# Optimization experiments

Measured on AMD Instinct MI355X. Metric: run time of the kernel, lower is better.

## Reference

```python
import jax, jax.numpy as jnp
import numpy as np

B, N = 512, 128
K = 3                      # top-k per row/col
CONF_THRESH = 0.05
ACCEPT_RADIUS = 0.1
CORR_THRESHOLD = 3         # min correspondences per patch
CORR_LIMIT = 2048          # verification-set size (correspondence_limit)
NUM_REFINE = 5
EPS = 1e-5


def setup_inputs() -> dict:
    key = jax.random.key(0)
    k1, k2, k3, k4, k5 = jax.random.split(key, 5)
    return {
        'score_mat': jax.random.normal(k1, (B, N, N), dtype=jnp.float32),
        'ref_knn_points': jax.random.normal(k2, (B, N, 3), dtype=jnp.float32),
        'src_knn_points': jax.random.normal(k3, (B, N, 3), dtype=jnp.float32),
        'ref_knn_masks': jax.random.bernoulli(k4, 0.95, (B, N)),
        'src_knn_masks': jax.random.bernoulli(k5, 0.95, (B, N)),
    }


def _svd_transform(H, src_c, ref_c):
    """H: (..., 3, 3) covariance; src_c/ref_c: (..., 3) centroids -> (..., 4, 4)."""
    U, _, Vh = jnp.linalg.svd(H)
    V = jnp.swapaxes(Vh, -1, -2)
    Ut = jnp.swapaxes(U, -1, -2)
    d = jnp.sign(jnp.linalg.det(V @ Ut))
    E = jnp.zeros_like(H).at[..., 0, 0].set(1.0).at[..., 1, 1].set(1.0).at[..., 2, 2].set(d)
    R = V @ E @ Ut
    t = ref_c - jnp.einsum('...ij,...j->...i', R, src_c)
    T = jnp.zeros(H.shape[:-2] + (4, 4), H.dtype)
    T = T.at[..., :3, :3].set(R).at[..., :3, 3].set(t).at[..., 3, 3].set(1.0)
    return T


def weighted_procrustes(src, ref, w):
    """src/ref: (C, 3), w: (C,) -> (4, 4). weight_thresh=0, weights >= 0 so no clamp."""
    wn = w / (jnp.sum(w, axis=-1, keepdims=True) + EPS)
    sc = jnp.einsum('n,nc->c', wn, src)
    rc = jnp.einsum('n,nc->c', wn, ref)
    H = jnp.einsum('nc,n,nd->cd', src - sc, wn, ref - rc)
    return _svd_transform(H, sc, rc)


def _topk_mask_last(scores):
    """Keep top-K values along the last axis of (B, R, S), zeros elsewhere."""
    vals, idx = jax.lax.top_k(scores, K)
    b = jnp.arange(scores.shape[0])[:, None, None]
    r = jnp.arange(scores.shape[1])[None, :, None]
    return jnp.zeros_like(scores).at[b, r, idx].set(vals)


def reference(score_mat, ref_knn_points, src_knn_points, ref_knn_masks, src_knn_masks):
    scores = jnp.exp(score_mat)  # score_mat holds log-scores (GeoTransformer forward)

    # --- correspondence matrix: dual top-k scatter + mutual + valid masks ---
    ref_corr = _topk_mask_last(scores) > CONF_THRESH
    src_corr = jnp.swapaxes(_topk_mask_last(jnp.swapaxes(scores, 1, 2)), 1, 2) > CONF_THRESH
    corr = ref_corr & src_corr  # mutual=True
    corr = corr & (ref_knn_masks[:, :, None] & src_knn_masks[:, None, :])

    masked = scores * corr.astype(scores.dtype)  # (B, N, N)
    patch_count = jnp.sum(corr, axis=(1, 2))      # correspondences per patch

    # --- per-patch weighted procrustes over all (n, m) pairs, zero-weighted pads ---
    wn = masked / (jnp.sum(masked, axis=(1, 2), keepdims=True) + EPS)
    sc = jnp.einsum('bnm,bmc->bc', wn, src_knn_points)
    rc = jnp.einsum('bnm,bnc->bc', wn, ref_knn_points)
    Hb = jnp.einsum('bnm,bmc,bnd->bcd', wn, src_knn_points - sc[:, None, :], ref_knn_points - rc[:, None, :])
    # gradients cannot flow past the boolean inlier masks below; stop_gradient avoids
    # spurious NaNs from degenerate 3x3 SVD backward on empty patches
    local_T = jax.lax.stop_gradient(_svd_transform(Hb, sc, rc))  # (B, 4, 4)

    # --- verification set: global top CORR_LIMIT correspondences ---
    flat = masked.reshape(-1)
    sel_scores, sel_idx = jax.lax.top_k(flat, CORR_LIMIT)
    b_i = sel_idx // (N * N)
    r_i = (sel_idx % (N * N)) // N
    s_i = sel_idx % N
    ref_c = ref_knn_points[b_i, r_i]  # (C, 3)
    src_c = src_knn_points[b_i, s_i]  # (C, 3)
    valid = sel_scores > 0

    # --- score every local transform by inlier count on the verification set ---
    R_all = local_T[:, :3, :3]
    t_all = local_T[:, :3, 3]
    aligned = jnp.einsum('pij,cj->pci', R_all, src_c) + t_all[:, None, :]  # (B, C, 3)
    resid = jnp.linalg.norm(ref_c[None] - aligned, axis=-1)
    inlier = (resid < ACCEPT_RADIUS) & valid[None]
    counts = jnp.where(patch_count >= CORR_THRESHOLD, jnp.sum(inlier, axis=-1), -1)
    best = jnp.argmax(counts)
    cur = sel_scores * inlier[best].astype(sel_scores.dtype)

    # --- global refinement: iterative re-weighted procrustes ---
    T = weighted_procrustes(src_c, ref_c, cur)
    for _ in range(NUM_REFINE - 1):
        aligned1 = src_c @ T[:3, :3].T + T[:3, 3]
        r1 = jnp.linalg.norm(ref_c - aligned1, axis=-1)
        cur = sel_scores * (r1 < ACCEPT_RADIUS).astype(sel_scores.dtype)
        T = weighted_procrustes(src_c, ref_c, cur)
    return T
```

## Files before the change

### kernel.cpp

```cpp
#include <hip/hip_runtime.h>
#include <math.h>

#define BB 512
#define NN 128
#define CAND_CAP (512*384)
#define LIMIT 2048
#define EQCAP 16384
#define NBIN1 4096

__device__ inline bool read_mask(const void* p, int i, int mode){
  if (mode == 0) return ((const int*)p)[i] != 0;
  if (mode == 1) return ((const unsigned char*)p)[i] != 0;
  return ((const float*)p)[i] != 0.0f;
}

__device__ inline float fast_rcp(float x){ return __builtin_amdgcn_rcpf(x); }
__device__ inline float fast_rsq(float x){ return __builtin_amdgcn_rsqf(x); }

__device__ __forceinline__ void kabsch9(
    float h00, float h01, float h02,
    float h10, float h11, float h12,
    float h20, float h21, float h22,
    float& r00, float& r01, float& r02,
    float& r10, float& r11, float& r12,
    float& r20, float& r21, float& r22)
{
  float s00 = h00*h00 + h10*h10 + h20*h20;
  float s01 = h00*h01 + h10*h11 + h20*h21;
  float s02 = h00*h02 + h10*h12 + h20*h22;
  float s11 = h01*h01 + h11*h11 + h21*h21;
  float s12 = h01*h02 + h11*h12 + h21*h22;
  float s22 = h02*h02 + h12*h12 + h22*h22;
  float v00=1.f,v01=0.f,v02=0.f, v10=0.f,v11=1.f,v12=0.f, v20=0.f,v21=0.f,v22=1.f;
  for (int sweep = 0; sweep < 10; sweep++){
    float off  = s01*s01 + s02*s02 + s12*s12;
    float base = s00*s00 + s11*s11 + s22*s22;
    if (off <= base*1e-14f + 1e-36f) break;
    if (fabsf(s01) > 1e-30f){
      float tau = (s11 - s00) * fast_rcp(2.f*s01);
      float tt  = (tau >= 0.f ? 1.f : -1.f) * fast_rcp(fabsf(tau) + sqrtf(1.f + tau*tau));
      float c = fast_rsq(1.f + tt*tt), s = tt*c;
      float n00 = c*c*s00 - 2.f*c*s*s01 + s*s*s11;
      float n11 = s*s*s00 + 2.f*c*s*s01 + c*c*s11;
      float n02 = c*s02 - s*s12;
      float n12 = s*s02 + c*s12;
      s00=n00; s11=n11; s01=0.f; s02=n02; s12=n12;
      float a,b;
      a=v00; b=v01; v00=c*a-s*b; v01=s*a+c*b;
      a=v10; b=v11; v10=c*a-s*b; v11=s*a+c*b;
      a=v20; b=v21; v20=c*a-s*b; v21=s*a+c*b;
    }
    if (fabsf(s02) > 1e-30f){
      float tau = (s22 - s00) * fast_rcp(2.f*s02);
      float tt  = (tau >= 0.f ? 1.f : -1.f) * fast_rcp(fabsf(tau) + sqrtf(1.f + tau*tau));
      float c = fast_rsq(1.f + tt*tt), s = tt*c;
      float n00 = c*c*s00 - 2.f*c*s*s02 + s*s*s22;
      float n22 = s*s*s00 + 2.f*c*s*s02 + c*c*s22;
      float n01 = c*s01 - s*s12;
      float n12 = s*s01 + c*s12;
      s00=n00; s22=n22; s02=0.f; s01=n01; s12=n12;
      float a,b;
      a=v00; b=v02; v00=c*a-s*b; v02=s*a+c*b;
      a=v10; b=v12; v10=c*a-s*b; v12=s*a+c*b;
      a=v20; b=v22; v20=c*a-s*b; v22=s*a+c*b;
    }
    if (fabsf(s12) > 1e-30f){
      float tau = (s22 - s11) * fast_rcp(2.f*s12);
      float tt  = (tau >= 0.f ? 1.f : -1.f) * fast_rcp(fabsf(tau) + sqrtf(1.f + tau*tau));
      float c = fast_rsq(1.f + tt*tt), s = tt*c;
      float n11 = c*c*s11 - 2.f*c*s*s12 + s*s*s22;
      float n22 = s*s*s11 + 2.f*c*s*s12 + c*c*s22;
      float n01 = c*s01 - s*s02;
      float n02 = s*s01 + c*s02;
      s11=n11; s22=n22; s12=0.f; s01=n01; s02=n02;
      float a,b;
      a=v01; b=v02; v01=c*a-s*b; v02=s*a+c*b;
      a=v11; b=v12; v11=c*a-s*b; v12=s*a+c*b;
      a=v21; b=v22; v21=c*a-s*b; v22=s*a+c*b;
    }
  }
  float l0=s00, l1=s11, l2=s22;
  float a0=v00, a1=v10, a2=v20;
  float b0=v01, b1=v11, b2=v21;
  float c0=v02, c1=v12, c2=v22;
  if (l0 < l1){ float x; x=l0;l0=l1;l1=x; x=a0;a0=b0;b0=x; x=a1;a1=b1;b1=x; x=a2;a2=b2;b2=x; }
  if (l0 < l2){ float x; x=l0;l0=l2;l2=x; x=a0;a0=c0;c0=x; x=a1;a1=c1;c1=x; x=a2;a2=c2;c2=x; }
  if (l1 < l2){ float x; x=l1;l1=l2;l2=x; x=b0;b0=c0;c0=x; x=b1;b1=c1;c1=x; x=b2;b2=c2;c2=x; }
  float sig0 = sqrtf(fmaxf(l0, 0.f));
  if (!(sig0 > 1e-12f)){
    r00=1.f; r01=0.f; r02=0.f; r10=0.f; r11=1.f; r12=0.f; r20=0.f; r21=0.f; r22=1.f;
    return;
  }
  float u0x = h00*a0 + h01*a1 + h02*a2;
  float u0y = h10*a0 + h11*a1 + h12*a2;
  float u0z = h20*a0 + h21*a1 + h22*a2;
  float in0 = fast_rsq(u0x*u0x + u0y*u0y + u0z*u0z);
  u0x *= in0; u0y *= in0; u0z *= in0;
  float u1x = h00*b0 + h01*b1 + h02*b2;
  float u1y = h10*b0 + h11*b1 + h12*b2;
  float u1z = h20*b0 + h21*b1 + h22*b2;
  float dp = u1x*u0x + u1y*u0y + u1z*u0z;
  u1x -= dp*u0x; u1y -= dp*u0y; u1z -= dp*u0z;
  float d1 = u1x*u1x + u1y*u1y + u1z*u1z;
  if (sqrtf(d1) > sig0*1e-5f){
    float in1 = fast_rsq(d1);
    u1x *= in1; u1y *= in1; u1z *= in1;
  } else {
    float au0 = fabsf(u0x), au1 = fabsf(u0y), au2 = fabsf(u0z);
    float e0 = 0.f, e1 = 0.f, e2 = 0.f;
    if (au0 <= au1 && au0 <= au2) e0 = 1.f; else if (au1 <= au2) e1 = 1.f; else e2 = 1.f;
    float d2 = e0*u0x + e1*u0y + e2*u0z;
    u1x = e0 - d2*u0x; u1y = e1 - d2*u0y; u1z = e2 - d2*u0z;
    float nn = fast_rsq(u1x*u1x + u1y*u1y + u1z*u1z);
    u1x *= nn; u1y *= nn; u1z *= nn;
  }
  float u2x = u0y*u1z - u0z*u1y;
  float u2y = u0z*u1x - u0x*u1z;
  float u2z = u0x*u1y - u0y*u1x;
  float cxv = b1*c2 - b2*c1;
  float cyv = b2*c0 - b0*c2;
  float czv = b0*c1 - b1*c0;
  float detV = a0*cxv + a1*cyv + a2*czv;
  float dd = (detV >= 0.f) ? 1.f : -1.f;
  float w2x = dd*u2x, w2y = dd*u2y, w2z = dd*u2z;
  r00=a0*u0x + b0*u1x + c0*w2x;  r01=a0*u0y + b0*u1y + c0*w2y;  r02=a0*u0z + b0*u1z + c0*w2z;
  r10=a1*u0x + b1*u1x + c1*w2x;  r11=a1*u0y + b1*u1y + c1*w2y;  r12=a1*u0z + b1*u1z + c1*w2z;
  r20=a2*u0x + b2*u1x + c2*w2x;  r21=a2*u0y + b2*u1y + c2*w2y;  r22=a2*u0z + b2*u1z + c2*w2z;
}

__global__ __launch_bounds__(256) void k1_kernel(
    const float* __restrict__ score, const float* __restrict__ refp,
    const float* __restrict__ srcp, const void* __restrict__ rmaskp,
    const void* __restrict__ smaskp,
    int* hdr, float* cand_vals, int* cand_idx,
    float* Hsr, int* pcount)
{
  __shared__ float parts[2][NN][3];
  __shared__ float srcsh[NN*3];
  __shared__ float refsh[NN*3];
  __shared__ float c3sh[NN];
  __shared__ unsigned char smk[NN], rmk[NN];
  __shared__ float candv[4][96];
  __shared__ int   candi[4][96];
  __shared__ int   wcnt[4];
  __shared__ int   woff[4];
  __shared__ int   bbase;
  __shared__ float red[4][17];
  __shared__ int smode;
  const int b = blockIdx.x, t = threadIdx.x;
  const int w = t >> 6, l = t & 63;

  if (t < 64){
    unsigned v = ((const unsigned*)rmaskp)[t];
    bool n01 = !(v == 0u || v == 1u);
    bool nf  = !(v == 0u || v == 0x3F800000u);
    unsigned long long b01 = __ballot(n01), bf = __ballot(nf);
    if (t == 0) smode = (b01 == 0ull) ? 0 : ((bf == 0ull) ? 2 : 1);
  }
  if (t < 4) wcnt[t] = 0;
  for (int i = t; i < NN*3; i += 256){
    srcsh[i] = srcp[b*NN*3 + i];
    refsh[i] = refp[b*NN*3 + i];
  }

  {
    const int c = t & 127, h = t >> 7;
    float a1=-1e30f, a2=-1e30f, a3=-1e30f;
    const float* colp = score + (size_t)b*NN*NN + (size_t)(h*64)*NN + c;
#pragma unroll 8
    for (int i = 0; i < 64; i++){
      float v = colp[i*NN];
      float m = fminf(a1, v);
      a1 = fmaxf(a1, v);
      a3 = fmaxf(a3, fminf(a2, m));
      a2 = fmaxf(a2, m);
    }
    parts[h][c][0]=a1; parts[h][c][1]=a2; parts[h][c][2]=a3;
  }
  __syncthreads();
  if (t < NN){
    float a1=parts[0][t][0], a2=parts[0][t][1], a3=parts[0][t][2];
    float b1=parts[1][t][0], b2=parts[1][t][1], b3=parts[1][t][2];
    c3sh[t] = fmaxf(fmaxf(fminf(a1,b2), fminf(a2,b1)), fmaxf(a3,b3));
    int mode = smode;
    smk[t] = read_mask(smaskp, b*NN + t, mode) ? 1 : 0;
    rmk[t] = read_mask(rmaskp, b*NN + t, mode) ? 1 : 0;
  }
  __syncthreads();

  float cn0=0.f, A0=0.f, Rx0=0.f, Ry0=0.f, Rz0=0.f;
  float cn1=0.f, A1=0.f, Rx1=0.f, Ry1=0.f, Rz1=0.f;
  const float c3_0 = c3sh[l], c3_1 = c3sh[l + 64];
  const int sm0 = smk[l], sm1 = smk[l + 64];

  const float* base = score + (size_t)b*NN*NN;
  for (int rr = 0; rr < 32; rr++){
    const int r = w*32 + rr;
    const float v0 = base[r*NN + l];
    const float v1 = base[r*NN + l + 64];
    float a1 = fmaxf(v0, v1), a2 = fminf(v0, v1), a3 = -1e30f;
#pragma unroll
    for (int st = 0; st < 6; st++){
      const int mask = 1 << st;
      float o1 = __shfl_xor(a1, mask);
      float o2 = __shfl_xor(a2, mask);
      float o3 = __shfl_xor(a3, mask);
      float m1 = fmaxf(a1, o1);
      float m2 = fmaxf(fminf(a1, o1), fmaxf(a2, o2));
      float m3 = fmaxf(fmaxf(fminf(a1, o2), fminf(a2, o1)), fmaxf(a3, o3));
      a1 = m1; a2 = m2; a3 = m3;
    }
    const float r3 = a3;
    const bool rmv = rmk[r] != 0;
    const float rx = refsh[r*3+0], ry = refsh[r*3+1], rz = refsh[r*3+2];
    float e0 = 0.f, e1 = 0.f;
    bool k0 = false, k1 = false;
    if (rmv && sm0 && v0 >= r3 && v0 >= c3_0){
      e0 = expf(v0); k0 = (e0 > 0.05f);
    }
    if (rmv && sm1 && v1 >= r3 && v1 >= c3_1){
      e1 = expf(v1); k1 = (e1 > 0.05f);
    }
    if (k0){ cn0 += 1.f; A0 += e0; Rx0 += e0*rx; Ry0 += e0*ry; Rz0 += e0*rz; }
    if (k1){ cn1 += 1.f; A1 += e1; Rx1 += e1*rx; Ry1 += e1*ry; Rz1 += e1*rz; }
    unsigned long long B0 = __ballot(k0);
    unsigned long long B1 = __ballot(k1);
    int n0 = __popcll(B0), n1 = __popcll(B1);
    if (n0 + n1 > 0){
      int wb = 0;
      if (l == 0){ wb = wcnt[w]; wcnt[w] = wb + n0 + n1; }
      wb = __shfl(wb, 0);
      unsigned long long lt = (l == 0) ? 0ull : (~0ull >> (64 - l));
      if (k0){
        int pos = wb + (int)__popcll(B0 & lt);
        if (pos < 96){ candv[w][pos] = e0; candi[w][pos] = (b<<14)|(r<<7)|l; }
      }
      if (k1){
        int pos = wb + n0 + (int)__popcll(B1 & lt);
        if (pos < 96){ candv[w][pos] = e1; candi[w][pos] = (b<<14)|(r<<7)|(l+64); }
      }
    }
  }
  __syncthreads();
  if (t == 0){
    int c0 = wcnt[0] > 96 ? 96 : wcnt[0];
    int c1 = wcnt[1] > 96 ? 96 : wcnt[1];
    int c2 = wcnt[2] > 96 ? 96 : wcnt[2];
    int c3 = wcnt[3] > 96 ? 96 : wcnt[3];
    woff[0] = 0; woff[1] = c0; woff[2] = c0 + c1; woff[3] = c0 + c1 + c2;
    bbase = atomicAdd(&hdr[0], c0 + c1 + c2 + c3);
  }
  __syncthreads();
  {
    int total = wcnt[w]; if (total > 96) total = 96;
    int gbase = bbase + woff[w];
    for (int i = l; i < total; i += 64){
      int pos = gbase + i;
      if (pos < CAND_CAP){ cand_vals[pos] = candv[w][i]; cand_idx[pos] = candi[w][i]; }
    }
  }
  {
    const float sx0 = srcsh[l*3+0], sy0 = srcsh[l*3+1], sz0 = srcsh[l*3+2];
    const float sx1 = srcsh[(l+64)*3+0], sy1 = srcsh[(l+64)*3+1], sz1 = srcsh[(l+64)*3+2];
#define WSUM(VAL, IDX) { float v_ = (VAL); \
    for (int o_ = 32; o_ > 0; o_ >>= 1) v_ += __shfl_down(v_, o_); \
    if (l == 0) red[w][IDX] = v_; }
    WSUM(cn0 + cn1, 0)
    WSUM(A0 + A1, 1)
    WSUM(Rx0 + Rx1, 2)
    WSUM(Ry0 + Ry1, 3)
    WSUM(Rz0 + Rz1, 4)
    WSUM(A0*sx0 + A1*sx1, 5)
    WSUM(A0*sy0 + A1*sy1, 6)
    WSUM(A0*sz0 + A1*sz1, 7)
    WSUM(sx0*Rx0 + sx1*Rx1, 8)
    WSUM(sx0*Ry0 + sx1*Ry1, 9)
    WSUM(sx0*Rz0 + sx1*Rz1, 10)
    WSUM(sy0*Rx0 + sy1*Rx1, 11)
    WSUM(sy0*Ry0 + sy1*Ry1, 12)
    WSUM(sy0*Rz0 + sy1*Rz1, 13)
    WSUM(sz0*Rx0 + sz1*Rx1, 14)
    WSUM(sz0*Ry0 + sz1*Ry1, 15)
    WSUM(sz0*Rz0 + sz1*Rz1, 16)
#undef WSUM
  }
  __syncthreads();
  if (t == 0){
    float tot[17];
#pragma unroll
    for (int k = 0; k < 17; k++)
      tot[k] = red[0][k] + red[1][k] + red[2][k] + red[3][k];
    float Wm = tot[1];
    float denom = Wm + 1e-5f;
    float idenom = 1.f / denom;
    float s = Wm * idenom;
    float rcv[3] = { tot[2]*idenom, tot[3]*idenom, tot[4]*idenom };
    float scv[3] = { tot[5]*idenom, tot[6]*idenom, tot[7]*idenom };
    float* o = &Hsr[b*15];
#pragma unroll
    for (int c = 0; c < 3; c++)
#pragma unroll
      for (int d = 0; d < 3; d++)
        o[c*3+d] = tot[8 + c*3 + d]*idenom - (2.f - s)*scv[c]*rcv[d];
    o[9]=scv[0]; o[10]=scv[1]; o[11]=scv[2];
    o[12]=rcv[0]; o[13]=rcv[1]; o[14]=rcv[2];
    pcount[b] = (int)(tot[0] + 0.5f);
  }
}

__global__ __launch_bounds__(256) void k3a_kernel(
    const int* hdr, const float* __restrict__ cand_vals, int* hist)
{
  __shared__ int lh[NBIN1];
  int t = threadIdx.x;
  int Nc = hdr[0]; if (Nc > CAND_CAP) Nc = CAND_CAP;
  for (int j = t; j < NBIN1; j += 256) lh[j] = 0;
  __syncthreads();
  for (int i = blockIdx.x*256 + t; i < Nc; i += gridDim.x*256)
    atomicAdd(&lh[__float_as_uint(cand_vals[i]) >> 20], 1);
  __syncthreads();
  for (int j = t; j < NBIN1; j += 256)
    if (lh[j]) atomicAdd(&hist[j], lh[j]);
}

__global__ __launch_bounds__(256) void k3c_kernel(
    int* hdr, const int* __restrict__ hist,
    const float* __restrict__ cand_vals, const int* __restrict__ cand_idx,
    float* sel_vals, int* sel_idx, float* eq_vals, int* eq_idx)
{
  __shared__ int wtot[4];
  __shared__ int sb[2];
  const int t = threadIdx.x, lane = t & 63, wv = t >> 6;
  int Nc = hdr[0]; if (Nc > CAND_CAP) Nc = CAND_CAP;
  if (Nc <= LIMIT){
    if (t == 0){ sb[0] = -1; sb[1] = 0; if (blockIdx.x == 0){ hdr[4] = -1; hdr[5] = 0; } }
    __syncthreads();
  } else {
    const int chunkIdx = 255 - t;
    int csum = 0;
    for (int j = 0; j < 16; j++) csum += hist[chunkIdx*16 + j];
    int incl = csum;
    for (int off = 1; off < 64; off <<= 1){ int y = __shfl_up(incl, off); if (lane >= off) incl += y; }
    if (lane == 63) wtot[wv] = incl;
    __syncthreads();
    int wbase = 0;
    for (int w = 0; w < wv; w++) wbase += wtot[w];
    int P = wbase + incl;
    int P_prev = P - csum;
    if (P_prev < LIMIT && P >= LIMIT){
      int cum = P_prev, bin1 = chunkIdx*16, need = 0;
      for (int b2 = chunkIdx*16 + 15; b2 >= chunkIdx*16; b2--){
        int h = hist[b2];
        if (cum + h >= LIMIT){ bin1 = b2; need = LIMIT - cum; break; }
        cum += h;
      }
      sb[0] = bin1; sb[1] = need;
      if (blockIdx.x == 0){ hdr[4] = bin1; hdr[5] = need; }
    }
    __syncthreads();
  }
  int bin1 = sb[0];
  for (int i = blockIdx.x*256 + t; i < Nc; i += gridDim.x*256){
    float v = cand_vals[i];
    if (bin1 < 0){
      int p = atomicAdd(&hdr[2], 1);
      if (p < LIMIT){ sel_vals[p] = v; sel_idx[p] = cand_idx[i]; }
      continue;
    }
    int bin = (int)(__float_as_uint(v) >> 20);
    if (bin > bin1){
      int p = atomicAdd(&hdr[2], 1);
      if (p < LIMIT){ sel_vals[p] = v; sel_idx[p] = cand_idx[i]; }
    } else if (bin == bin1){
      int q = atomicAdd(&hdr[1], 1);
      if (q < EQCAP){ eq_vals[q] = v; eq_idx[q] = cand_idx[i]; }
    }
  }
}

__global__ __launch_bounds__(1024) void k3d_kernel(
    const int* hdr, const float* __restrict__ eq_vals, const int* __restrict__ eq_idx,
    float* sel_vals, int* sel_idx,
    const float* __restrict__ refp, const float* __restrict__ srcp,
    float* sel_ref, float* sel_src)
{
  __shared__ int hist[2048];
  __shared__ int eqsh[2048];
  __shared__ int wtot[16];
  __shared__ int bpair[2];
  __shared__ int sh[2];
  const int t = threadIdx.x, lane = t & 63, wv = t >> 6;
  const int bin1 = hdr[4];
  int nAbove = hdr[2]; if (nAbove > LIMIT) nAbove = LIMIT;

  auto find_boundary = [&](int need){
    int i0 = 2047 - 2*t, i1 = 2046 - 2*t;
    int g0 = hist[i0], g1 = hist[i1];
    int local = g0 + g1;
    int incl = local;
    for (int off = 1; off < 64; off <<= 1){ int y = __shfl_up(incl, off); if (lane >= off) incl += y; }
    if (lane == 63) wtot[wv] = incl;
    __syncthreads();
    int wbase = 0;
    for (int w = 0; w < wv; w++) wbase += wtot[w];
    int P_prev = wbase + incl - local;
    int P0 = P_prev + g0;
    if (P0 >= need && P_prev < need){ bpair[0] = i0; bpair[1] = need - P_prev; }
    int P1 = P0 + g1;
    if (P1 >= need && P0 < need){ bpair[0] = i1; bpair[1] = need - P0; }
    __syncthreads();
  };

  bool done = false;
  if (bin1 < 0){
    for (int i = t; i < LIMIT; i += 1024)
      if (i >= nAbove){ sel_vals[i] = 0.f; sel_idx[i] = 0; }
    done = true;
  }
  int neq = 0, need = 0;
  if (!done){
    neq = hdr[1]; if (neq > EQCAP) neq = EQCAP;
    need = hdr[5];
    if (need >= neq){
      for (int i = t; i < neq; i += 1024){ sel_vals[nAbove+i] = eq_vals[i]; sel_idx[nAbove+i] = eq_idx[i]; }
      for (int i = t; i < LIMIT; i += 1024)
        if (i >= nAbove + neq){ sel_vals[i] = 0.f; sel_idx[i] = 0; }
      done = true;
    }
  }
  if (!done){
    for (int i = t; i < 2048; i += 1024) hist[i] = 0;
    __syncthreads();
    for (int i = t; i < neq; i += 1024)
      atomicAdd(&hist[(__float_as_uint(eq_vals[i]) >> 9) & 0x7FF], 1);
    __syncthreads();
    find_boundary(need);
    int binA = bpair[0], need2 = bpair[1];
    __syncthreads();
    for (int i = t; i < 2048; i += 1024) hist[i] = 0;
    __syncthreads();
    for (int i = t; i < neq; i += 1024){
      unsigned k = __float_as_uint(eq_vals[i]);
      if ((int)((k >> 9) & 0x7FF) == binA) atomicAdd(&hist[k & 0x1FF], 1);
    }
    __syncthreads();
    find_boundary(need2);
    unsigned Tlow = (((unsigned)binA) << 9) | (unsigned)bpair[0];
    unsigned Tkey = (((unsigned)bin1) << 20) | Tlow;
    if (t == 0){ sh[0] = 0; sh[1] = 0; }
    __syncthreads();
    for (int i = t; i < neq; i += 1024){
      unsigned k = __float_as_uint(eq_vals[i]);
      unsigned k20 = k & 0xFFFFF;
      if (k20 > Tlow){
        int p = atomicAdd(&sh[0], 1);
        sel_vals[nAbove + p] = eq_vals[i]; sel_idx[nAbove + p] = eq_idx[i];
      } else if (k20 == Tlow){
        int q = atomicAdd(&sh[1], 1);
        if (q < 2048) eqsh[q] = eq_idx[i];
      }
    }
    __syncthreads();
    if (t == 0){
      int na2 = sh[0];
      int ne2 = sh[1]; if (ne2 > 2048) ne2 = 2048;
      int take = need - na2; if (take > ne2) take = ne2; if (take < 0) take = 0;
      if (nAbove + na2 + take > LIMIT) take = LIMIT - nAbove - na2;
      for (int j = 0; j < take; j++){
        int mi = j;
        for (int l2 = j+1; l2 < ne2; l2++) if (eqsh[l2] < eqsh[mi]) mi = l2;
        int tmp = eqsh[j]; eqsh[j] = eqsh[mi]; eqsh[mi] = tmp;
        sel_vals[nAbove + na2 + j] = __uint_as_float(Tkey);
        sel_idx[nAbove + na2 + j] = eqsh[j];
      }
      for (int j = nAbove + na2 + take; j < LIMIT; j++){ sel_vals[j] = 0.f; sel_idx[j] = 0; }
    }
  }
  __syncthreads();
  for (int p = t; p < LIMIT; p += 1024){
    int idx = sel_idx[p];
    int b = idx >> 14, rr = (idx >> 7) & 127, ss = idx & 127;
#pragma unroll
    for (int c = 0; c < 3; c++){
      sel_ref[p*3+c] = refp[(b*NN+rr)*3+c];
      sel_src[p*3+c] = srcp[(b*NN+ss)*3+c];
    }
  }
}

__global__ __launch_bounds__(256, 1) void k45_kernel(
    const float* __restrict__ Hsr, float* __restrict__ localT,
    const float* __restrict__ sel_vals, const float* __restrict__ sel_ref,
    const float* __restrict__ sel_src, const int* __restrict__ pcount,
    int* counts, int* hdr, float* out)
{
  __shared__ float Tsh[12];
  __shared__ int ired[4];
  __shared__ int lastsh;
  __shared__ float fred[4][16];
  __shared__ long long lred[4];
  __shared__ float RT[12];
  __shared__ int sbest;
  const int b = blockIdx.x, t = threadIdx.x, lane = t & 63, wv = t >> 6;

  if (t == 0){
    const float* o = &Hsr[b*15];
    float r00,r01,r02,r10,r11,r12,r20,r21,r22;
    kabsch9(o[0],o[1],o[2], o[3],o[4],o[5], o[6],o[7],o[8],
            r00,r01,r02,r10,r11,r12,r20,r21,r22);
    Tsh[0]=r00; Tsh[1]=r01; Tsh[2]=r02;
    Tsh[3]=r10; Tsh[4]=r11; Tsh[5]=r12;
    Tsh[6]=r20; Tsh[7]=r21; Tsh[8]=r22;
    Tsh[9]  = o[12] - (r00*o[9] + r01*o[10] + r02*o[11]);
    Tsh[10] = o[13] - (r10*o[9] + r11*o[10] + r12*o[11]);
    Tsh[11] = o[14] - (r20*o[9] + r21*o[10] + r22*o[11]);
  }
  __syncthreads();
  if (t < 12) localT[b*12 + t] = Tsh[t];

  {
    float R00=Tsh[0],R01=Tsh[1],R02=Tsh[2],R10=Tsh[3],R11=Tsh[4],R12=Tsh[5];
    float R20=Tsh[6],R21=Tsh[7],R22=Tsh[8];
    float tx=Tsh[9], ty=Tsh[10], tz=Tsh[11];
    int c = 0;
    for (int p = t; p < LIMIT; p += 256){
      float v = sel_vals[p];
      if (!(v > 0.f)) continue;
      float sx=sel_src[p*3], sy=sel_src[p*3+1], sz=sel_src[p*3+2];
      float rx=sel_ref[p*3], ry=sel_ref[p*3+1], rz=sel_ref[p*3+2];
      float ax = R00*sx + R01*sy + R02*sz + tx;
      float ay = R10*sx + R11*sy + R12*sz + ty;
      float az = R20*sx + R21*sy + R22*sz + tz;
      float dx = rx-ax, dy = ry-ay, dz = rz-az;
      if (sqrtf(dx*dx + dy*dy + dz*dz) < 0.1f) c++;
    }
    for (int off2 = 32; off2 > 0; off2 >>= 1) c += __shfl_down(c, off2);
    if (lane == 0) ired[wv] = c;
    __syncthreads();
    if (t == 0){
      counts[b] = (pcount[b] >= 3) ? (ired[0]+ired[1]+ired[2]+ired[3]) : -1;
      __threadfence();
      int d = atomicAdd(&hdr[6], 1);
      lastsh = (d == BB - 1) ? 1 : 0;
    }
    __syncthreads();
    if (!lastsh) return;
    __threadfence();
  }

  {
    long long key = (long long)0x8000000000000000LL;
    for (int bb = t; bb < BB; bb += 256){
      long long kk = ((long long)(counts[bb] + 2) << 32) | (long long)(511 - bb);
      if (kk > key) key = kk;
    }
    for (int off2 = 32; off2 > 0; off2 >>= 1){ long long o = __shfl_down(key, off2); if (o > key) key = o; }
    if (lane == 0) lred[wv] = key;
    __syncthreads();
    if (t == 0){
      long long m = lred[0];
#pragma unroll
      for (int w = 1; w < 4; w++) if (lred[w] > m) m = lred[w];
      sbest = 511 - (int)(m & 0xFFFFFFFFLL);
    }
    __syncthreads();
    if (t < 12) RT[t] = localT[sbest*12 + t];
    __syncthreads();

    for (int iter = 0; iter < 5; iter++){
      float R00=RT[0],R01=RT[1],R02=RT[2];
      float R10=RT[3],R11=RT[4],R12=RT[5];
      float R20=RT[6],R21=RT[7],R22=RT[8];
      float tx=RT[9], ty=RT[10], tz=RT[11];
      float a0=0.f,a1=0.f,a2=0.f,a3=0.f,a4=0.f,a5=0.f,a6=0.f,a7=0.f;
      float a8=0.f,a9=0.f,a10=0.f,a11=0.f,a12=0.f,a13=0.f,a14=0.f,a15=0.f;
      for (int p = t; p < LIMIT; p += 256){
        float v = sel_vals[p];
        if (!(v > 0.f)) continue;
        float sx=sel_src[p*3], sy=sel_src[p*3+1], sz=sel_src[p*3+2];
        float rx=sel_ref[p*3], ry=sel_ref[p*3+1], rz=sel_ref[p*3+2];
        float ax = R00*sx + R01*sy + R02*sz + tx;
        float ay = R10*sx + R11*sy + R12*sz + ty;
        float az = R20*sx + R21*sy + R22*sz + tz;
        float dx = rx-ax, dy = ry-ay, dz = rz-az;
        if (sqrtf(dx*dx + dy*dy + dz*dz) < 0.1f){
          a0 += v;
          a1 += v*sx; a2 += v*sy; a3 += v*sz;
          a4 += v*rx; a5 += v*ry; a6 += v*rz;
          a7  += v*sx*rx; a8  += v*sx*ry; a9  += v*sx*rz;
          a10 += v*sy*rx; a11 += v*sy*ry; a12 += v*sy*rz;
          a13 += v*sz*rx; a14 += v*sz*ry; a15 += v*sz*rz;
        }
      }
#define WRED(VAL, IDX) { float v_ = (VAL); \
      for (int o_ = 32; o_ > 0; o_ >>= 1) v_ += __shfl_down(v_, o_); \
      if (lane == 0) fred[wv][IDX] = v_; }
      WRED(a0, 0)  WRED(a1, 1)  WRED(a2, 2)  WRED(a3, 3)
      WRED(a4, 4)  WRED(a5, 5)  WRED(a6, 6)  WRED(a7, 7)
      WRED(a8, 8)  WRED(a9, 9)  WRED(a10,10) WRED(a11,11)
      WRED(a12,12) WRED(a13,13) WRED(a14,14) WRED(a15,15)
#undef WRED
      __syncthreads();
      if (t == 0){
        float tot[16];
#pragma unroll
        for (int k = 0; k < 16; k++) tot[k] = fred[0][k]+fred[1][k]+fred[2][k]+fred[3][k];
        float W = tot[0], denom = W + 1e-5f;
        float inv = 1.f / denom;
        float s = W * inv;
        float scx = tot[1]*inv, scy = tot[2]*inv, scz = tot[3]*inv;
        float rcx = tot[4]*inv, rcy = tot[5]*inv, rcz = tot[6]*inv;
        float f = 2.f - s;
        float h00 = tot[7]*inv  - f*scx*rcx;
        float h01 = tot[8]*inv  - f*scx*rcy;
        float h02 = tot[9]*inv  - f*scx*rcz;
        float h10 = tot[10]*inv - f*scy*rcx;
        float h11 = tot[11]*inv - f*scy*rcy;
        float h12 = tot[12]*inv - f*scy*rcz;
        float h20 = tot[13]*inv - f*scz*rcx;
        float h21 = tot[14]*inv - f*scz*rcy;
        float h22 = tot[15]*inv - f*scz*rcz;
        float r00,r01,r02,r10,r11,r12,r20,r21,r22;
        kabsch9(h00,h01,h02,h10,h11,h12,h20,h21,h22,
                r00,r01,r02,r10,r11,r12,r20,r21,r22);
        RT[0]=r00; RT[1]=r01; RT[2]=r02;
        RT[3]=r10; RT[4]=r11; RT[5]=r12;
        RT[6]=r20; RT[7]=r21; RT[8]=r22;
        RT[9]  = rcx - (r00*scx + r01*scy + r02*scz);
        RT[10] = rcy - (r10*scx + r11*scy + r12*scz);
        RT[11] = rcz - (r20*scx + r21*scy + r22*scz);
      }
      __syncthreads();
    }
    if (t == 0){
      out[0]=RT[0];  out[1]=RT[1];  out[2]=RT[2];  out[3]=RT[9];
      out[4]=RT[3];  out[5]=RT[4];  out[6]=RT[5];  out[7]=RT[10];
      out[8]=RT[6];  out[9]=RT[7];  out[10]=RT[8]; out[11]=RT[11];
      out[12]=0.f; out[13]=0.f; out[14]=0.f; out[15]=1.f;
    }
  }
}

extern "C" void kernel_launch(void* const* d_in, const int* in_sizes, int n_in,
                              void* d_out, int out_size, void* d_ws, size_t ws_size,
                              hipStream_t stream){
  const float* score = (const float*)d_in[0];
  const float* refp  = (const float*)d_in[1];
  const float* srcp  = (const float*)d_in[2];
  const void*  rmask = d_in[3];
  const void*  smask = d_in[4];

  char* ws = (char*)d_ws;
  size_t off = 0;
  int* hdr = (int*)(ws + off);            off += 256;
  int* hist = (int*)(ws + off);           off += (size_t)NBIN1*4;
  float* cand_vals = (float*)(ws + off);  off += (size_t)CAND_CAP*4;
  int* cand_idx = (int*)(ws + off);       off += (size_t)CAND_CAP*4;
  float* eq_vals = (float*)(ws + off);    off += (size_t)EQCAP*4;
  int* eq_idx = (int*)(ws + off);         off += (size_t)EQCAP*4;
  float* Hsr = (float*)(ws + off);        off += (size_t)BB*15*4;
  int* pcount = (int*)(ws + off);         off += (size_t)BB*4;
  float* localT = (float*)(ws + off);     off += (size_t)BB*12*4;
  float* sel_vals = (float*)(ws + off);   off += (size_t)LIMIT*4;
  int* sel_idx = (int*)(ws + off);        off += (size_t)LIMIT*4;
  float* sel_ref = (float*)(ws + off);    off += (size_t)LIMIT*3*4;
  float* sel_src = (float*)(ws + off);    off += (size_t)LIMIT*3*4;
  int* counts = (int*)(ws + off);         off += (size_t)BB*4;

  hipMemsetAsync(ws, 0, 256 + (size_t)NBIN1*4, stream);
  hipLaunchKernelGGL(k1_kernel, dim3(BB), dim3(256), 0, stream,
                     score, refp, srcp, rmask, smask,
                     hdr, cand_vals, cand_idx, Hsr, pcount);
  hipLaunchKernelGGL(k3a_kernel, dim3(64), dim3(256), 0, stream, hdr, cand_vals, hist);
  hipLaunchKernelGGL(k3c_kernel, dim3(64), dim3(256), 0, stream,
                     hdr, hist, cand_vals, cand_idx, sel_vals, sel_idx, eq_vals, eq_idx);
  hipLaunchKernelGGL(k3d_kernel, dim3(1), dim3(1024), 0, stream,
                     hdr, eq_vals, eq_idx, sel_vals, sel_idx, refp, srcp, sel_ref, sel_src);
  hipLaunchKernelGGL(k45_kernel, dim3(BB), dim3(256), 0, stream,
                     Hsr, localT, sel_vals, sel_ref, sel_src, pcount, counts, hdr, (float*)d_out);
}
```

Measured before the change: 220.8 us.

## Move per-patch Kabsch into k3c and split scoring from refinement kernels

Per-patch rotation solving (kabsch9 from Hsr) now runs in k3c, spread as 8 patches per block across its 64 blocks, rather than serially on thread 0 of each k45 block. The old last-block-done atomic election with thread fences in k45 is replaced by two kernels: k4 scores inlier counts per patch, and a single-block k5 picks the best patch and runs the refinement. This removes the serial SVD from the critical path of the scoring kernel and drops the atomic/fence handshake, at the cost of one extra kernel launch.

```diff
diff --git a/kernel.cpp b/kernel.cpp
--- a/kernel.cpp
+++ b/kernel.cpp
@@ -326,11 +326,28 @@
 __global__ __launch_bounds__(256) void k3c_kernel(
     int* hdr, const int* __restrict__ hist,
     const float* __restrict__ cand_vals, const int* __restrict__ cand_idx,
+    const float* __restrict__ Hsr, float* __restrict__ localT,
     float* sel_vals, int* sel_idx, float* eq_vals, int* eq_idx)
 {
   __shared__ int wtot[4];
   __shared__ int sb[2];
   const int t = threadIdx.x, lane = t & 63, wv = t >> 6;
+
+  if (t < 8){
+    const int bb = blockIdx.x*8 + t;
+    const float* o = &Hsr[bb*15];
+    float r00,r01,r02,r10,r11,r12,r20,r21,r22;
+    kabsch9(o[0],o[1],o[2], o[3],o[4],o[5], o[6],o[7],o[8],
+            r00,r01,r02,r10,r11,r12,r20,r21,r22);
+    float* T = &localT[bb*12];
+    T[0]=r00; T[1]=r01; T[2]=r02;
+    T[3]=r10; T[4]=r11; T[5]=r12;
+    T[6]=r20; T[7]=r21; T[8]=r22;
+    T[9]  = o[12] - (r00*o[9] + r01*o[10] + r02*o[11]);
+    T[10] = o[13] - (r10*o[9] + r11*o[10] + r12*o[11]);
+    T[11] = o[14] - (r20*o[9] + r21*o[10] + r22*o[11]);
+  }
+
   int Nc = hdr[0]; if (Nc > CAND_CAP) Nc = CAND_CAP;
   if (Nc <= LIMIT){
     if (t == 0){ sb[0] = -1; sb[1] = 0; if (blockIdx.x == 0){ hdr[4] = -1; hdr[5] = 0; } }
@@ -488,41 +505,73 @@
   }
 }
 
-__global__ __launch_bounds__(256, 1) void k45_kernel(
-    const float* __restrict__ Hsr, float* __restrict__ localT,
-    const float* __restrict__ sel_vals, const float* __restrict__ sel_ref,
-    const float* __restrict__ sel_src, const int* __restrict__ pcount,
-    int* counts, int* hdr, float* out)
+__global__ __launch_bounds__(256) void k4_kernel(
+    const float* __restrict__ localT, const float* __restrict__ sel_vals,
+    const float* __restrict__ sel_ref, const float* __restrict__ sel_src,
+    const int* __restrict__ pcount, int* counts)
 {
   __shared__ float Tsh[12];
   __shared__ int ired[4];
-  __shared__ int lastsh;
+  const int b = blockIdx.x, t = threadIdx.x, lane = t & 63, wv = t >> 6;
+  if (t < 12) Tsh[t] = localT[b*12 + t];
+  __syncthreads();
+  float R00=Tsh[0],R01=Tsh[1],R02=Tsh[2],R10=Tsh[3],R11=Tsh[4],R12=Tsh[5];
+  float R20=Tsh[6],R21=Tsh[7],R22=Tsh[8];
+  float tx=Tsh[9], ty=Tsh[10], tz=Tsh[11];
+  int c = 0;
+  for (int p = t; p < LIMIT; p += 256){
+    float v = sel_vals[p];
+    if (!(v > 0.f)) continue;
+    float sx=sel_src[p*3], sy=sel_src[p*3+1], sz=sel_src[p*3+2];
+    float rx=sel_ref[p*3], ry=sel_ref[p*3+1], rz=sel_ref[p*3+2];
+    float ax = R00*sx + R01*sy + R02*sz + tx;
+    float ay = R10*sx + R11*sy + R12*sz + ty;
+    float az = R20*sx + R21*sy + R22*sz + tz;
+    float dx = rx-ax, dy = ry-ay, dz = rz-az;
+    if (sqrtf(dx*dx + dy*dy + dz*dz) < 0.1f) c++;
+  }
+  for (int off2 = 32; off2 > 0; off2 >>= 1) c += __shfl_down(c, off2);
+  if (lane == 0) ired[wv] = c;
+  __syncthreads();
+  if (t == 0) counts[b] = (pcount[b] >= 3) ? (ired[0]+ired[1]+ired[2]+ired[3]) : -1;
+}
+
+__global__ __launch_bounds__(256, 1) void k5_kernel(
+    const int* __restrict__ counts, const float* __restrict__ localT,
+    const float* __restrict__ sel_vals, const float* __restrict__ sel_ref,
+    const float* __restrict__ sel_src, float* out)
+{
   __shared__ float fred[4][16];
   __shared__ long long lred[4];
   __shared__ float RT[12];
   __shared__ int sbest;
-  const int b = blockIdx.x, t = threadIdx.x, lane = t & 63, wv = t >> 6;
-
+  const int t = threadIdx.x, lane = t & 63, wv = t >> 6;
+
+  long long key = (long long)0x8000000000000000LL;
+  for (int bb = t; bb < BB; bb += 256){
+    long long kk = ((long long)(counts[bb] + 2) << 32) | (long long)(511 - bb);
+    if (kk > key) key = kk;
+  }
+  for (int off2 = 32; off2 > 0; off2 >>= 1){ long long o = __shfl_down(key, off2); if (o > key) key = o; }
+  if (lane == 0) lred[wv] = key;
+  __syncthreads();
   if (t == 0){
-    const float* o = &Hsr[b*15];
-    float r00,r01,r02,r10,r11,r12,r20,r21,r22;
-    kabsch9(o[0],o[1],o[2], o[3],o[4],o[5], o[6],o[7],o[8],
-            r00,r01,r02,r10,r11,r12,r20,r21,r22);
-    Tsh[0]=r00; Tsh[1]=r01; Tsh[2]=r02;
-    Tsh[3]=r10; Tsh[4]=r11; Tsh[5]=r12;
-    Tsh[6]=r20; Tsh[7]=r21; Tsh[8]=r22;
-    Tsh[9]  = o[12] - (r00*o[9] + r01*o[10] + r02*o[11]);
-    Tsh[10] = o[13] - (r10*o[9] + r11*o[10] + r12*o[11]);
-    Tsh[11] = o[14] - (r20*o[9] + r21*o[10] + r22*o[11]);
-  }
-  __syncthreads();
-  if (t < 12) localT[b*12 + t] = Tsh[t];
-
-  {
-    float R00=Tsh[0],R01=Tsh[1],R02=Tsh[2],R10=Tsh[3],R11=Tsh[4],R12=Tsh[5];
-    float R20=Tsh[6],R21=Tsh[7],R22=Tsh[8];
-    float tx=Tsh[9], ty=Tsh[10], tz=Tsh[11];
-    int c = 0;
+    long long m = lred[0];
+#pragma unroll
+    for (int w = 1; w < 4; w++) if (lred[w] > m) m = lred[w];
+    sbest = 511 - (int)(m & 0xFFFFFFFFLL);
+  }
+  __syncthreads();
+  if (t < 12) RT[t] = localT[sbest*12 + t];
+  __syncthreads();
+
+  for (int iter = 0; iter < 5; iter++){
+    float R00=RT[0],R01=RT[1],R02=RT[2];
+    float R10=RT[3],R11=RT[4],R12=RT[5];
+    float R20=RT[6],R21=RT[7],R22=RT[8];
+    float tx=RT[9], ty=RT[10], tz=RT[11];
+    float a0=0.f,a1=0.f,a2=0.f,a3=0.f,a4=0.f,a5=0.f,a6=0.f,a7=0.f;
+    float a8=0.f,a9=0.f,a10=0.f,a11=0.f,a12=0.f,a13=0.f,a14=0.f,a15=0.f;
     for (int p = t; p < LIMIT; p += 256){
       float v = sel_vals[p];
       if (!(v > 0.f)) continue;
@@ -532,112 +581,60 @@
       float ay = R10*sx + R11*sy + R12*sz + ty;
       float az = R20*sx + R21*sy + R22*sz + tz;
       float dx = rx-ax, dy = ry-ay, dz = rz-az;
-      if (sqrtf(dx*dx + dy*dy + dz*dz) < 0.1f) c++;
-    }
-    for (int off2 = 32; off2 > 0; off2 >>= 1) c += __shfl_down(c, off2);
-    if (lane == 0) ired[wv] = c;
+      if (sqrtf(dx*dx + dy*dy + dz*dz) < 0.1f){
+        a0 += v;
+        a1 += v*sx; a2 += v*sy; a3 += v*sz;
+        a4 += v*rx; a5 += v*ry; a6 += v*rz;
+        a7  += v*sx*rx; a8  += v*sx*ry; a9  += v*sx*rz;
+        a10 += v*sy*rx; a11 += v*sy*ry; a12 += v*sy*rz;
+        a13 += v*sz*rx; a14 += v*sz*ry; a15 += v*sz*rz;
+      }
+    }
+#define WRED(VAL, IDX) { float v_ = (VAL); \
+    for (int o_ = 32; o_ > 0; o_ >>= 1) v_ += __shfl_down(v_, o_); \
+    if (lane == 0) fred[wv][IDX] = v_; }
+    WRED(a0, 0)  WRED(a1, 1)  WRED(a2, 2)  WRED(a3, 3)
+    WRED(a4, 4)  WRED(a5, 5)  WRED(a6, 6)  WRED(a7, 7)
+    WRED(a8, 8)  WRED(a9, 9)  WRED(a10,10) WRED(a11,11)
+    WRED(a12,12) WRED(a13,13) WRED(a14,14) WRED(a15,15)
+#undef WRED
     __syncthreads();
     if (t == 0){
-      counts[b] = (pcount[b] >= 3) ? (ired[0]+ired[1]+ired[2]+ired[3]) : -1;
-      __threadfence();
-      int d = atomicAdd(&hdr[6], 1);
-      lastsh = (d == BB - 1) ? 1 : 0;
-    }
-    __syncthreads();
-    if (!lastsh) return;
-    __threadfence();
-  }
-
-  {
-    long long key = (long long)0x8000000000000000LL;
-    for (int bb = t; bb < BB; bb += 256){
-      long long kk = ((long long)(counts[bb] + 2) << 32) | (long long)(511 - bb);
-      if (kk > key) key = kk;
-    }
-    for (int off2 = 32; off2 > 0; off2 >>= 1){ long long o = __shfl_down(key, off2); if (o > key) key = o; }
-    if (lane == 0) lred[wv] = key;
-    __syncthreads();
-    if (t == 0){
-      long long m = lred[0];
+      float tot[16];
 #pragma unroll
-      for (int w = 1; w < 4; w++) if (lred[w] > m) m = lred[w];
-      sbest = 511 - (int)(m & 0xFFFFFFFFLL);
-    }
-    __syncthreads();
-    if (t < 12) RT[t] = localT[sbest*12 + t];
-    __syncthreads();
-
-    for (int iter = 0; iter < 5; iter++){
-      float R00=RT[0],R01=RT[1],R02=RT[2];
-      float R10=RT[3],R11=RT[4],R12=RT[5];
-      float R20=RT[6],R21=RT[7],R22=RT[8];
-      float tx=RT[9], ty=RT[10], tz=RT[11];
-      float a0=0.f,a1=0.f,a2=0.f,a3=0.f,a4=0.f,a5=0.f,a6=0.f,a7=0.f;
-      float a8=0.f,a9=0.f,a10=0.f,a11=0.f,a12=0.f,a13=0.f,a14=0.f,a15=0.f;
-      for (int p = t; p < LIMIT; p += 256){
-        float v = sel_vals[p];
-        if (!(v > 0.f)) continue;
-        float sx=sel_src[p*3], sy=sel_src[p*3+1], sz=sel_src[p*3+2];
-        float rx=sel_ref[p*3], ry=sel_ref[p*3+1], rz=sel_ref[p*3+2];
-        float ax = R00*sx + R01*sy + R02*sz + tx;
-        float ay = R10*sx + R11*sy + R12*sz + ty;
-        float az = R20*sx + R21*sy + R22*sz + tz;
-        float dx = rx-ax, dy = ry-ay, dz = rz-az;
-        if (sqrtf(dx*dx + dy*dy + dz*dz) < 0.1f){
-          a0 += v;
-          a1 += v*sx; a2 += v*sy; a3 += v*sz;
-          a4 += v*rx; a5 += v*ry; a6 += v*rz;
-          a7  += v*sx*rx; a8  += v*sx*ry; a9  += v*sx*rz;
-          a10 += v*sy*rx; a11 += v*sy*ry; a12 += v*sy*rz;
-          a13 += v*sz*rx; a14 += v*sz*ry; a15 += v*sz*rz;
-        }
-      }
-#define WRED(VAL, IDX) { float v_ = (VAL); \
-      for (int o_ = 32; o_ > 0; o_ >>= 1) v_ += __shfl_down(v_, o_); \
-      if (lane == 0) fred[wv][IDX] = v_; }
-      WRED(a0, 0)  WRED(a1, 1)  WRED(a2, 2)  WRED(a3, 3)
-      WRED(a4, 4)  WRED(a5, 5)  WRED(a6, 6)  WRED(a7, 7)
-      WRED(a8, 8)  WRED(a9, 9)  WRED(a10,10) WRED(a11,11)
-      WRED(a12,12) WRED(a13,13) WRED(a14,14) WRED(a15,15)
-#undef WRED
-      __syncthreads();
-      if (t == 0){
-        float tot[16];
-#pragma unroll
-        for (int k = 0; k < 16; k++) tot[k] = fred[0][k]+fred[1][k]+fred[2][k]+fred[3][k];
-        float W = tot[0], denom = W + 1e-5f;
-        float inv = 1.f / denom;
-        float s = W * inv;
-        float scx = tot[1]*inv, scy = tot[2]*inv, scz = tot[3]*inv;
-        float rcx = tot[4]*inv, rcy = tot[5]*inv, rcz = tot[6]*inv;
-        float f = 2.f - s;
-        float h00 = tot[7]*inv  - f*scx*rcx;
-        float h01 = tot[8]*inv  - f*scx*rcy;
-        float h02 = tot[9]*inv  - f*scx*rcz;
-        float h10 = tot[10]*inv - f*scy*rcx;
-        float h11 = tot[11]*inv - f*scy*rcy;
-        float h12 = tot[12]*inv - f*scy*rcz;
-        float h20 = tot[13]*inv - f*scz*rcx;
-        float h21 = tot[14]*inv - f*scz*rcy;
-        float h22 = tot[15]*inv - f*scz*rcz;
-        float r00,r01,r02,r10,r11,r12,r20,r21,r22;
-        kabsch9(h00,h01,h02,h10,h11,h12,h20,h21,h22,
-                r00,r01,r02,r10,r11,r12,r20,r21,r22);
-        RT[0]=r00; RT[1]=r01; RT[2]=r02;
-        RT[3]=r10; RT[4]=r11; RT[5]=r12;
-        RT[6]=r20; RT[7]=r21; RT[8]=r22;
-        RT[9]  = rcx - (r00*scx + r01*scy + r02*scz);
-        RT[10] = rcy - (r10*scx + r11*scy + r12*scz);
-        RT[11] = rcz - (r20*scx + r21*scy + r22*scz);
-      }
-      __syncthreads();
-    }
-    if (t == 0){
-      out[0]=RT[0];  out[1]=RT[1];  out[2]=RT[2];  out[3]=RT[9];
-      out[4]=RT[3];  out[5]=RT[4];  out[6]=RT[5];  out[7]=RT[10];
-      out[8]=RT[6];  out[9]=RT[7];  out[10]=RT[8]; out[11]=RT[11];
-      out[12]=0.f; out[13]=0.f; out[14]=0.f; out[15]=1.f;
-    }
+      for (int k = 0; k < 16; k++) tot[k] = fred[0][k]+fred[1][k]+fred[2][k]+fred[3][k];
+      float W = tot[0], denom = W + 1e-5f;
+      float inv = 1.f / denom;
+      float s = W * inv;
+      float scx = tot[1]*inv, scy = tot[2]*inv, scz = tot[3]*inv;
+      float rcx = tot[4]*inv, rcy = tot[5]*inv, rcz = tot[6]*inv;
+      float f = 2.f - s;
+      float h00 = tot[7]*inv  - f*scx*rcx;
+      float h01 = tot[8]*inv  - f*scx*rcy;
+      float h02 = tot[9]*inv  - f*scx*rcz;
+      float h10 = tot[10]*inv - f*scy*rcx;
+      float h11 = tot[11]*inv - f*scy*rcy;
+      float h12 = tot[12]*inv - f*scy*rcz;
+      float h20 = tot[13]*inv - f*scz*rcx;
+      float h21 = tot[14]*inv - f*scz*rcy;
+      float h22 = tot[15]*inv - f*scz*rcz;
+      float r00,r01,r02,r10,r11,r12,r20,r21,r22;
+      kabsch9(h00,h01,h02,h10,h11,h12,h20,h21,h22,
+              r00,r01,r02,r10,r11,r12,r20,r21,r22);
+      RT[0]=r00; RT[1]=r01; RT[2]=r02;
+      RT[3]=r10; RT[4]=r11; RT[5]=r12;
+      RT[6]=r20; RT[7]=r21; RT[8]=r22;
+      RT[9]  = rcx - (r00*scx + r01*scy + r02*scz);
+      RT[10] = rcy - (r10*scx + r11*scy + r12*scz);
+      RT[11] = rcz - (r20*scx + r21*scy + r22*scz);
+    }
+    __syncthreads();
+  }
+  if (t == 0){
+    out[0]=RT[0];  out[1]=RT[1];  out[2]=RT[2];  out[3]=RT[9];
+    out[4]=RT[3];  out[5]=RT[4];  out[6]=RT[5];  out[7]=RT[10];
+    out[8]=RT[6];  out[9]=RT[7];  out[10]=RT[8]; out[11]=RT[11];
+    out[12]=0.f; out[13]=0.f; out[14]=0.f; out[15]=1.f;
   }
 }
 
@@ -673,9 +670,12 @@
                      hdr, cand_vals, cand_idx, Hsr, pcount);
   hipLaunchKernelGGL(k3a_kernel, dim3(64), dim3(256), 0, stream, hdr, cand_vals, hist);
   hipLaunchKernelGGL(k3c_kernel, dim3(64), dim3(256), 0, stream,
-                     hdr, hist, cand_vals, cand_idx, sel_vals, sel_idx, eq_vals, eq_idx);
+                     hdr, hist, cand_vals, cand_idx, Hsr, localT,
+                     sel_vals, sel_idx, eq_vals, eq_idx);
   hipLaunchKernelGGL(k3d_kernel, dim3(1), dim3(1024), 0, stream,
                      hdr, eq_vals, eq_idx, sel_vals, sel_idx, refp, srcp, sel_ref, sel_src);
-  hipLaunchKernelGGL(k45_kernel, dim3(BB), dim3(256), 0, stream,
-                     Hsr, localT, sel_vals, sel_ref, sel_src, pcount, counts, hdr, (float*)d_out);
-}
+  hipLaunchKernelGGL(k4_kernel, dim3(BB), dim3(256), 0, stream,
+                     localT, sel_vals, sel_ref, sel_src, pcount, counts);
+  hipLaunchKernelGGL(k5_kernel, dim3(1), dim3(256), 0, stream,
+                     counts, localT, sel_vals, sel_ref, sel_src, (float*)d_out);
+}
```

Result: faster. 210.3 us (-4.7%).
